# Kernel tuning notes

Hardware: AMD Instinct MI355X
Metric: run time of the kernel (lower is better)

The kernel has to match this reference:

```python
import jax, jax.numpy as jnp
import numpy as np

T, H, O = 32768, 1024, 1024

def setup_inputs() -> dict:
    key = jax.random.key(0)
    k0, k1, k2 = jax.random.split(key, 3)
    dec_h = jax.random.normal(k0, (1, O), dtype=jnp.float32)
    enc = jax.random.normal(k1, (T, 1, H), dtype=jnp.float32)
    attn_w = jax.random.normal(k2, (1, O + H), dtype=jnp.float32) * 0.02
    attn_b = jnp.zeros((1,), dtype=jnp.float32)
    return {"dec_h": dec_h, "enc": enc, "attn_w": attn_w, "attn_b": attn_b}

def reference(dec_h, enc, attn_w, attn_b):
    # dec_h: [1, O]; enc: [T, 1, H]; attn_w: [1, O+H] (cat order: dec then enc)
    t, _, h = enc.shape
    o = dec_h.shape[1]
    enc2d = enc.reshape(t, h)                     # [T, H]
    w_dec = attn_w[:, :o]                         # [1, O]
    w_enc = attn_w[:, o:]                         # [1, H]
    # per-timestep Bahdanau score, vectorized over T
    scores = enc2d @ w_enc.T + (dec_h @ w_dec.T + attn_b)  # [T,1] + [1,1] -> [T,1]
    normalized_weights = jax.nn.softmax(scores.reshape(1, t), axis=1)  # [1, T]
    output = normalized_weights @ enc2d           # [1, H]
    return output, normalized_weights
```

## Files before the change

kernel.cpp:

```cpp
#include <hip/hip_runtime.h>
#include <hip/hip_bf16.h>

constexpr int T = 32768;
constexpr int H = 1024;

constexpr int NB1 = 1024;
constexpr int RPB = T / NB1;
constexpr int CH  = 8;

constexpr int MB_OFF  = 256;
constexpr int LB_OFF  = MB_OFF + NB1;
constexpr int SC_OFF  = 4096;
constexpr int ACC_OFF = SC_OFF + T;

__global__ __launch_bounds__(256) void fused_pass1(
    const float* __restrict__ enc, const float* __restrict__ w_enc,
    float* __restrict__ scores, float* __restrict__ mb, float* __restrict__ lb,
    float* __restrict__ accs, float* __restrict__ out) {
    const int b    = blockIdx.x;
    const int tid  = threadIdx.x;
    const int wave = tid >> 6;
    const int lane = tid & 63;
    const int row0 = b * RPB;

    if (b < 4) out[b * 256 + tid] = 0.f;

    const float4 w4 = *reinterpret_cast<const float4*>(w_enc + 4 * tid);

    __shared__ float red[4][CH];

    float  m = -1e30f, l = 0.f;
    float4 acc = make_float4(0.f, 0.f, 0.f, 0.f);

    for (int c = 0; c < RPB / CH; ++c) {
        const int r0 = row0 + c * CH;
        float4 e[CH];
        float  p[CH];
#pragma unroll
        for (int r = 0; r < CH; ++r) {
            e[r] = *reinterpret_cast<const float4*>(enc + (size_t)(r0 + r) * H + 4 * tid);
            p[r] = e[r].x * w4.x + e[r].y * w4.y + e[r].z * w4.z + e[r].w * w4.w;
        }
#pragma unroll
        for (int r = 0; r < CH; ++r) {
#pragma unroll
            for (int off = 32; off; off >>= 1) p[r] += __shfl_xor(p[r], off);
        }
        if (lane == 0) {
#pragma unroll
            for (int r = 0; r < CH; ++r) red[wave][r] = p[r];
        }
        __syncthreads();
        float s[CH];
        float mc = -1e30f;
#pragma unroll
        for (int r = 0; r < CH; ++r) {
            s[r] = red[0][r] + red[1][r] + red[2][r] + red[3][r];
            mc = fmaxf(mc, s[r]);
        }
        __syncthreads();

        const float mn  = fmaxf(m, mc);
        const float rs  = __expf(m - mn);
        l *= rs;
        acc.x *= rs; acc.y *= rs; acc.z *= rs; acc.w *= rs;
#pragma unroll
        for (int r = 0; r < CH; ++r) {
            const float wgt = __expf(s[r] - mn);
            l += wgt;
            acc.x = fmaf(wgt, e[r].x, acc.x);
            acc.y = fmaf(wgt, e[r].y, acc.y);
            acc.z = fmaf(wgt, e[r].z, acc.z);
            acc.w = fmaf(wgt, e[r].w, acc.w);
        }
        m = mn;

        if (tid == 0) {
#pragma unroll
            for (int r = 0; r < CH; ++r) scores[r0 + r] = s[r];
        }
    }

    *reinterpret_cast<float4*>(accs + (size_t)b * H + 4 * tid) = acc;
    if (tid == 0) { mb[b] = m; lb[b] = l; }
}

__global__ __launch_bounds__(256) void combine2(
    const float* __restrict__ mb, const float* __restrict__ lb,
    const float* __restrict__ accs, const float* __restrict__ scores,
    float* __restrict__ out, float* __restrict__ wout) {
    __shared__ float sm[8];
    const int tid  = threadIdx.x;
    const int wave = tid >> 6;
    const int lane = tid & 63;

    float m = fmaxf(fmaxf(mb[tid], mb[tid + 256]),
                    fmaxf(mb[tid + 512], mb[tid + 768]));
#pragma unroll
    for (int off = 32; off; off >>= 1) m = fmaxf(m, __shfl_xor(m, off));
    if (lane == 0) sm[wave] = m;
    __syncthreads();
    const float M = fmaxf(fmaxf(sm[0], sm[1]), fmaxf(sm[2], sm[3]));

    float l = lb[tid]       * __expf(mb[tid]       - M)
            + lb[tid + 256] * __expf(mb[tid + 256] - M)
            + lb[tid + 512] * __expf(mb[tid + 512] - M)
            + lb[tid + 768] * __expf(mb[tid + 768] - M);
#pragma unroll
    for (int off = 32; off; off >>= 1) l += __shfl_xor(l, off);
    if (lane == 0) sm[4 + wave] = l;
    __syncthreads();
    const float rL = 1.f / (sm[4] + sm[5] + sm[6] + sm[7]);

    if (blockIdx.x < 64) {
        const int b0 = blockIdx.x * 16;
        float4 a = make_float4(0.f, 0.f, 0.f, 0.f);
#pragma unroll 4
        for (int i = 0; i < 16; ++i) {
            const float wsc = __expf(mb[b0 + i] - M) * rL;
            float4 v = *reinterpret_cast<const float4*>(accs + (size_t)(b0 + i) * H + 4 * tid);
            a.x = fmaf(wsc, v.x, a.x);
            a.y = fmaf(wsc, v.y, a.y);
            a.z = fmaf(wsc, v.z, a.z);
            a.w = fmaf(wsc, v.w, a.w);
        }
        atomicAdd(&out[4 * tid + 0], a.x);
        atomicAdd(&out[4 * tid + 1], a.y);
        atomicAdd(&out[4 * tid + 2], a.z);
        atomicAdd(&out[4 * tid + 3], a.w);
    } else {
        const int t0 = (blockIdx.x - 64) * 1024 + 4 * tid;
        float4 sv = *reinterpret_cast<const float4*>(scores + t0);
        float4 wv;
        wv.x = __expf(sv.x - M) * rL;
        wv.y = __expf(sv.y - M) * rL;
        wv.z = __expf(sv.z - M) * rL;
        wv.w = __expf(sv.w - M) * rL;
        *reinterpret_cast<float4*>(wout + t0) = wv;
    }
}

extern "C" void kernel_launch(void* const* d_in, const int* in_sizes, int n_in,
                              void* d_out, int out_size, void* d_ws, size_t ws_size,
                              hipStream_t stream) {
    const float* enc    = (const float*)d_in[1];
    const float* attn_w = (const float*)d_in[2];
    const float* w_enc  = attn_w + 1024;

    float* out  = (float*)d_out;
    float* wout = (float*)d_out + H;

    float* ws     = (float*)d_ws;
    float* mb     = ws + MB_OFF;
    float* lb     = ws + LB_OFF;
    float* scores = ws + SC_OFF;
    float* accs   = ws + ACC_OFF;

    fused_pass1<<<NB1, 256, 0, stream>>>(enc, w_enc, scores, mb, lb, accs, out);
    combine2<<<96, 256, 0, stream>>>(mb, lb, accs, scores, out, wout);
}
```

Measured before the change: 208.5 us.

## Give each wave its own rows to drop block barriers in pass1

Each wave now processes whole rows independently, 8 rows per wave, and does the dot product with a wave-level shuffle reduction. This removes the shared-memory reduction and the two __syncthreads per chunk. Online softmax is updated per row with a branch that rescales only when a new max appears. In exchange, the partial accumulators grow from 1024 to 4096 rows, which quadruples the partial writes and the reads in combine, and combine is resized to 128 plus 32 blocks. There is also less memory-level parallelism per wave than in the 8-row batched loads.

```diff
diff --git a/kernel.cpp b/kernel.cpp
--- a/kernel.cpp
+++ b/kernel.cpp
@@ -4,139 +4,131 @@
 constexpr int T = 32768;
 constexpr int H = 1024;
 
-constexpr int NB1 = 1024;
-constexpr int RPB = T / NB1;
-constexpr int CH  = 8;
+constexpr int NW  = 4096;
+constexpr int RPW = T / NW;
+constexpr int NB1 = NW / 4;
 
-constexpr int MB_OFF  = 256;
-constexpr int LB_OFF  = MB_OFF + NB1;
-constexpr int SC_OFF  = 4096;
-constexpr int ACC_OFF = SC_OFF + T;
+constexpr int MW_OFF   = 0;
+constexpr int LW_OFF   = NW;
+constexpr int SC_OFF   = 2 * NW;
+constexpr int PART_OFF = 2 * NW + T;
 
-__global__ __launch_bounds__(256) void fused_pass1(
+__global__ __launch_bounds__(256) void pass1(
     const float* __restrict__ enc, const float* __restrict__ w_enc,
-    float* __restrict__ scores, float* __restrict__ mb, float* __restrict__ lb,
-    float* __restrict__ accs, float* __restrict__ out) {
-    const int b    = blockIdx.x;
-    const int tid  = threadIdx.x;
-    const int wave = tid >> 6;
-    const int lane = tid & 63;
-    const int row0 = b * RPB;
+    float* __restrict__ scores, float* __restrict__ mw, float* __restrict__ lw,
+    float* __restrict__ parts, float* __restrict__ out) {
+    const int tid   = threadIdx.x;
+    const int lane  = tid & 63;
+    const int gwave = blockIdx.x * 4 + (tid >> 6);
+    const int row0  = gwave * RPW;
 
-    if (b < 4) out[b * 256 + tid] = 0.f;
+    if (blockIdx.x < 4) out[blockIdx.x * 256 + tid] = 0.f;
 
-    const float4 w4 = *reinterpret_cast<const float4*>(w_enc + 4 * tid);
+    float4 w[4];
+#pragma unroll
+    for (int p = 0; p < 4; ++p)
+        w[p] = *reinterpret_cast<const float4*>(w_enc + p * 256 + lane * 4);
 
-    __shared__ float red[4][CH];
+    float  m = -3.0e38f, l = 0.f;
+    float4 acc[4];
+#pragma unroll
+    for (int p = 0; p < 4; ++p) acc[p] = make_float4(0.f, 0.f, 0.f, 0.f);
 
-    float  m = -1e30f, l = 0.f;
-    float4 acc = make_float4(0.f, 0.f, 0.f, 0.f);
+#pragma unroll 2
+    for (int r = 0; r < RPW; ++r) {
+        const float* rp = enc + (size_t)(row0 + r) * H;
+        float4 e[4];
+#pragma unroll
+        for (int p = 0; p < 4; ++p)
+            e[p] = *reinterpret_cast<const float4*>(rp + p * 256 + lane * 4);
 
-    for (int c = 0; c < RPB / CH; ++c) {
-        const int r0 = row0 + c * CH;
-        float4 e[CH];
-        float  p[CH];
+        float s = 0.f;
 #pragma unroll
-        for (int r = 0; r < CH; ++r) {
-            e[r] = *reinterpret_cast<const float4*>(enc + (size_t)(r0 + r) * H + 4 * tid);
-            p[r] = e[r].x * w4.x + e[r].y * w4.y + e[r].z * w4.z + e[r].w * w4.w;
+        for (int p = 0; p < 4; ++p)
+            s += e[p].x * w[p].x + e[p].y * w[p].y + e[p].z * w[p].z + e[p].w * w[p].w;
+#pragma unroll
+        for (int off = 32; off; off >>= 1) s += __shfl_xor(s, off);
+
+        if (lane == 0) scores[row0 + r] = s;
+
+        if (s > m) {
+            const float rs = __expf(m - s);
+            l *= rs;
+#pragma unroll
+            for (int p = 0; p < 4; ++p) {
+                acc[p].x *= rs; acc[p].y *= rs; acc[p].z *= rs; acc[p].w *= rs;
+            }
+            m = s;
         }
+        const float wgt = __expf(s - m);
+        l += wgt;
 #pragma unroll
-        for (int r = 0; r < CH; ++r) {
-#pragma unroll
-            for (int off = 32; off; off >>= 1) p[r] += __shfl_xor(p[r], off);
-        }
-        if (lane == 0) {
-#pragma unroll
-            for (int r = 0; r < CH; ++r) red[wave][r] = p[r];
-        }
-        __syncthreads();
-        float s[CH];
-        float mc = -1e30f;
-#pragma unroll
-        for (int r = 0; r < CH; ++r) {
-            s[r] = red[0][r] + red[1][r] + red[2][r] + red[3][r];
-            mc = fmaxf(mc, s[r]);
-        }
-        __syncthreads();
-
-        const float mn  = fmaxf(m, mc);
-        const float rs  = __expf(m - mn);
-        l *= rs;
-        acc.x *= rs; acc.y *= rs; acc.z *= rs; acc.w *= rs;
-#pragma unroll
-        for (int r = 0; r < CH; ++r) {
-            const float wgt = __expf(s[r] - mn);
-            l += wgt;
-            acc.x = fmaf(wgt, e[r].x, acc.x);
-            acc.y = fmaf(wgt, e[r].y, acc.y);
-            acc.z = fmaf(wgt, e[r].z, acc.z);
-            acc.w = fmaf(wgt, e[r].w, acc.w);
-        }
-        m = mn;
-
-        if (tid == 0) {
-#pragma unroll
-            for (int r = 0; r < CH; ++r) scores[r0 + r] = s[r];
+        for (int p = 0; p < 4; ++p) {
+            acc[p].x = fmaf(wgt, e[p].x, acc[p].x);
+            acc[p].y = fmaf(wgt, e[p].y, acc[p].y);
+            acc[p].z = fmaf(wgt, e[p].z, acc[p].z);
+            acc[p].w = fmaf(wgt, e[p].w, acc[p].w);
         }
     }
 
-    *reinterpret_cast<float4*>(accs + (size_t)b * H + 4 * tid) = acc;
-    if (tid == 0) { mb[b] = m; lb[b] = l; }
+#pragma unroll
+    for (int p = 0; p < 4; ++p)
+        *reinterpret_cast<float4*>(parts + (size_t)gwave * H + p * 256 + lane * 4) = acc[p];
+    if (lane == 0) { mw[gwave] = m; lw[gwave] = l; }
 }
 
-__global__ __launch_bounds__(256) void combine2(
-    const float* __restrict__ mb, const float* __restrict__ lb,
-    const float* __restrict__ accs, const float* __restrict__ scores,
+__global__ __launch_bounds__(256) void combine(
+    const float* __restrict__ mw, const float* __restrict__ lw,
+    const float* __restrict__ parts, const float* __restrict__ scores,
     float* __restrict__ out, float* __restrict__ wout) {
     __shared__ float sm[8];
     const int tid  = threadIdx.x;
-    const int wave = tid >> 6;
+    const int wv   = tid >> 6;
     const int lane = tid & 63;
 
-    float m = fmaxf(fmaxf(mb[tid], mb[tid + 256]),
-                    fmaxf(mb[tid + 512], mb[tid + 768]));
+    float m = -3.0e38f;
+#pragma unroll 4
+    for (int i = tid; i < NW; i += 256) m = fmaxf(m, mw[i]);
 #pragma unroll
     for (int off = 32; off; off >>= 1) m = fmaxf(m, __shfl_xor(m, off));
-    if (lane == 0) sm[wave] = m;
+    if (lane == 0) sm[wv] = m;
     __syncthreads();
     const float M = fmaxf(fmaxf(sm[0], sm[1]), fmaxf(sm[2], sm[3]));
 
-    float l = lb[tid]       * __expf(mb[tid]       - M)
-            + lb[tid + 256] * __expf(mb[tid + 256] - M)
-            + lb[tid + 512] * __expf(mb[tid + 512] - M)
-            + lb[tid + 768] * __expf(mb[tid + 768] - M);
+    float l = 0.f;
+#pragma unroll 4
+    for (int i = tid; i < NW; i += 256) l += lw[i] * __expf(mw[i] - M);
 #pragma unroll
     for (int off = 32; off; off >>= 1) l += __shfl_xor(l, off);
-    if (lane == 0) sm[4 + wave] = l;
+    if (lane == 0) sm[4 + wv] = l;
     __syncthreads();
     const float rL = 1.f / (sm[4] + sm[5] + sm[6] + sm[7]);
 
-    if (blockIdx.x < 64) {
-        const int b0 = blockIdx.x * 16;
+    if (blockIdx.x < 128) {
+        const int w0 = blockIdx.x * 32;
         float4 a = make_float4(0.f, 0.f, 0.f, 0.f);
 #pragma unroll 4
-        for (int i = 0; i < 16; ++i) {
-            const float wsc = __expf(mb[b0 + i] - M) * rL;
-            float4 v = *reinterpret_cast<const float4*>(accs + (size_t)(b0 + i) * H + 4 * tid);
-            a.x = fmaf(wsc, v.x, a.x);
-            a.y = fmaf(wsc, v.y, a.y);
-            a.z = fmaf(wsc, v.z, a.z);
-            a.w = fmaf(wsc, v.w, a.w);
+        for (int i = 0; i < 32; ++i) {
+            const float c = __expf(mw[w0 + i] - M) * rL;
+            float4 v = *reinterpret_cast<const float4*>(parts + (size_t)(w0 + i) * H + tid * 4);
+            a.x = fmaf(c, v.x, a.x);
+            a.y = fmaf(c, v.y, a.y);
+            a.z = fmaf(c, v.z, a.z);
+            a.w = fmaf(c, v.w, a.w);
         }
         atomicAdd(&out[4 * tid + 0], a.x);
         atomicAdd(&out[4 * tid + 1], a.y);
         atomicAdd(&out[4 * tid + 2], a.z);
         atomicAdd(&out[4 * tid + 3], a.w);
     } else {
-        const int t0 = (blockIdx.x - 64) * 1024 + 4 * tid;
+        const int t0 = (blockIdx.x - 128) * 1024 + 4 * tid;
         float4 sv = *reinterpret_cast<const float4*>(scores + t0);
-        float4 wv;
-        wv.x = __expf(sv.x - M) * rL;
-        wv.y = __expf(sv.y - M) * rL;
-        wv.z = __expf(sv.z - M) * rL;
-        wv.w = __expf(sv.w - M) * rL;
-        *reinterpret_cast<float4*>(wout + t0) = wv;
+        float4 wvout;
+        wvout.x = __expf(sv.x - M) * rL;
+        wvout.y = __expf(sv.y - M) * rL;
+        wvout.z = __expf(sv.z - M) * rL;
+        wvout.w = __expf(sv.w - M) * rL;
+        *reinterpret_cast<float4*>(wout + t0) = wvout;
     }
 }
 
@@ -151,11 +143,11 @@
     float* wout = (float*)d_out + H;
 
     float* ws     = (float*)d_ws;
-    float* mb     = ws + MB_OFF;
-    float* lb     = ws + LB_OFF;
+    float* mw     = ws + MW_OFF;
+    float* lw     = ws + LW_OFF;
     float* scores = ws + SC_OFF;
-    float* accs   = ws + ACC_OFF;
+    float* parts  = ws + PART_OFF;
 
-    fused_pass1<<<NB1, 256, 0, stream>>>(enc, w_enc, scores, mb, lb, accs, out);
-    combine2<<<96, 256, 0, stream>>>(mb, lb, accs, scores, out, wout);
+    pass1<<<NB1, 256, 0, stream>>>(enc, w_enc, scores, mw, lw, parts, out);
+    combine<<<160, 256, 0, stream>>>(mw, lw, parts, scores, out, wout);
 }
```

Result: slower. 219.6 us (+5.3%).

## Prefetch next chunk of encoder rows and double-buffer the reduction scratch

Applied to the files above, without the earlier changes.

The pass-1 kernel now loads the next 8 encoder rows into registers while it computes on the current chunk, so global loads overlap the shuffle reduction and softmax update. The shared reduction buffer is double-buffered by chunk parity, which lets one of the two block barriers per iteration be removed. Launch bounds also request 4 blocks per SM. The costs are higher register pressure from the extra float4 buffers, which could lower occupancy or cause spills, and a slightly different initial max sentinel.

```diff
diff --git a/kernel.cpp b/kernel.cpp
--- a/kernel.cpp
+++ b/kernel.cpp
@@ -7,13 +7,14 @@
 constexpr int NB1 = 1024;
 constexpr int RPB = T / NB1;
 constexpr int CH  = 8;
+constexpr int NCH = RPB / CH;
 
 constexpr int MB_OFF  = 256;
 constexpr int LB_OFF  = MB_OFF + NB1;
 constexpr int SC_OFF  = 4096;
 constexpr int ACC_OFF = SC_OFF + T;
 
-__global__ __launch_bounds__(256) void fused_pass1(
+__global__ __launch_bounds__(256, 4) void fused_pass1(
     const float* __restrict__ enc, const float* __restrict__ w_enc,
     float* __restrict__ scores, float* __restrict__ mb, float* __restrict__ lb,
     float* __restrict__ accs, float* __restrict__ out) {
@@ -27,20 +28,28 @@
 
     const float4 w4 = *reinterpret_cast<const float4*>(w_enc + 4 * tid);
 
-    __shared__ float red[4][CH];
+    __shared__ float red[2][4][CH];
 
-    float  m = -1e30f, l = 0.f;
+    float  m = -3.0e38f, l = 0.f;
     float4 acc = make_float4(0.f, 0.f, 0.f, 0.f);
 
-    for (int c = 0; c < RPB / CH; ++c) {
-        const int r0 = row0 + c * CH;
-        float4 e[CH];
-        float  p[CH];
+    float4 e[CH], en[CH];
 #pragma unroll
-        for (int r = 0; r < CH; ++r) {
-            e[r] = *reinterpret_cast<const float4*>(enc + (size_t)(r0 + r) * H + 4 * tid);
+    for (int r = 0; r < CH; ++r)
+        e[r] = *reinterpret_cast<const float4*>(enc + (size_t)(row0 + r) * H + 4 * tid);
+
+    for (int c = 0; c < NCH; ++c) {
+        if (c + 1 < NCH) {
+            const int rn = row0 + (c + 1) * CH;
+#pragma unroll
+            for (int r = 0; r < CH; ++r)
+                en[r] = *reinterpret_cast<const float4*>(enc + (size_t)(rn + r) * H + 4 * tid);
+        }
+
+        float p[CH];
+#pragma unroll
+        for (int r = 0; r < CH; ++r)
             p[r] = e[r].x * w4.x + e[r].y * w4.y + e[r].z * w4.z + e[r].w * w4.w;
-        }
 #pragma unroll
         for (int r = 0; r < CH; ++r) {
 #pragma unroll
@@ -48,20 +57,20 @@
         }
         if (lane == 0) {
 #pragma unroll
-            for (int r = 0; r < CH; ++r) red[wave][r] = p[r];
-        }
-        __syncthreads();
-        float s[CH];
-        float mc = -1e30f;
-#pragma unroll
-        for (int r = 0; r < CH; ++r) {
-            s[r] = red[0][r] + red[1][r] + red[2][r] + red[3][r];
-            mc = fmaxf(mc, s[r]);
+            for (int r = 0; r < CH; ++r) red[c & 1][wave][r] = p[r];
         }
         __syncthreads();
 
-        const float mn  = fmaxf(m, mc);
-        const float rs  = __expf(m - mn);
+        float s[CH];
+        float mc = -3.0e38f;
+#pragma unroll
+        for (int r = 0; r < CH; ++r) {
+            s[r] = red[c & 1][0][r] + red[c & 1][1][r] + red[c & 1][2][r] + red[c & 1][3][r];
+            mc = fmaxf(mc, s[r]);
+        }
+
+        const float mn = fmaxf(m, mc);
+        const float rs = __expf(m - mn);
         l *= rs;
         acc.x *= rs; acc.y *= rs; acc.z *= rs; acc.w *= rs;
 #pragma unroll
@@ -77,7 +86,12 @@
 
         if (tid == 0) {
 #pragma unroll
-            for (int r = 0; r < CH; ++r) scores[r0 + r] = s[r];
+            for (int r = 0; r < CH; ++r) scores[row0 + c * CH + r] = s[r];
+        }
+
+        if (c + 1 < NCH) {
+#pragma unroll
+            for (int r = 0; r < CH; ++r) e[r] = en[r];
         }
     }
 
```

New measurement: 220.5 us. 1.06x slower.
